# Kernel tuning notes

Measured on AMD Instinct MI355X. Metric: run time of the kernel, lower is better.

The kernel has to match this reference:

```python
import jax, jax.numpy as jnp
import numpy as np

N_NODES = 100000
N_EDGES = 6400000
C = 1.0      # LJ energy scale
R_C = 1.0    # LJ length scale
P = 12
Q = 6
GAMMA = 0.1  # velocity damping
MIN_R = 0.1  # distance clamp
EPS = 1e-12  # torch F.normalize eps
BOX = 100.0  # position domain scale


def setup_inputs() -> dict:
    key = jax.random.key(0)
    k1, k2, k3, k4 = jax.random.split(key, 4)
    x = jax.random.uniform(k1, (N_NODES, 2), dtype=jnp.float32) * BOX
    v = jax.random.normal(k2, (N_NODES, 2), dtype=jnp.float32)
    edge_src = jax.random.randint(k3, (N_EDGES,), 0, N_NODES, dtype=jnp.int64)
    edge_dst = jax.random.randint(k4, (N_EDGES,), 0, N_NODES, dtype=jnp.int64)
    return {"x": x, "v": v, "edge_src": edge_src, "edge_dst": edge_dst}


def lj_force(r_in):
    # r clamped below at MIN_R, matching r*(r>min_r) + min_r*(r<=min_r)
    r = jnp.where(r_in > MIN_R, r_in, MIN_R)
    s = R_C / r
    return 4.0 * C * s**Q * (P * s**(P - Q) - Q) / r


def reference(x, v, edge_src, edge_dst):
    # gather: dr = dst_pos - src_pos (non-periodic euclid distance vector)
    dr = x[edge_dst] - x[edge_src]                       # [E,2]
    abs_dr = jnp.linalg.norm(dr, axis=-1, keepdims=True)  # [E,1]
    unit_dr = dr / jnp.maximum(abs_dr, EPS)               # F.normalize
    msg = lj_force(abs_dr) * unit_dr                      # [E,2]
    # scatter-sum messages to destination nodes
    acc = jax.ops.segment_sum(msg, edge_dst, num_segments=N_NODES)  # [N,2]
    acc = acc - GAMMA * v
    return acc
```

## Files before the change

### kernel.cpp

```cpp
#include <hip/hip_runtime.h>


constexpr float GAMMA = 0.1f;
constexpr float MIN_R = 0.1f;
constexpr float EPSN  = 1e-12f;

constexpr int NPB   = 128;
constexpr int NBPAD = 1024;
constexpr int CHUNK = 16384;
constexpr int STHREADS = 512;
constexpr int K     = CHUNK / STHREADS;
constexpr int CAPB  = 8960;
constexpr unsigned INVALID = 0xFFFFFFFFu;

__device__ __forceinline__ float2 lj_msg(float2 xs, float2 xd) {
    float dx = xd.x - xs.x;
    float dy = xd.y - xs.y;
    float ab = sqrtf(dx * dx + dy * dy);
    float r  = ab > MIN_R ? ab : MIN_R;
    float inv = 1.0f / r;
    float s2 = inv * inv;
    float s6 = s2 * s2 * s2;
    float f  = 4.0f * s6 * (12.0f * s6 - 6.0f) * inv;
    float c  = f / fmaxf(ab, EPSN);
    return make_float2(c * dx, c * dy);
}

__global__ __launch_bounds__(256) void zero_kernel(unsigned* __restrict__ p, int n) {
    int i = blockIdx.x * blockDim.x + threadIdx.x;
    if (i < n) p[i] = 0u;
}

__global__ __launch_bounds__(STHREADS, 2) void scatter_kernel(
    const int4* __restrict__ src4, const int4* __restrict__ dst4,
    unsigned* __restrict__ records, unsigned* __restrict__ gcur,
    int nE, int NB)
{
    __shared__ unsigned sorted[CHUNK];
    __shared__ unsigned cnt[NBPAD];
    __shared__ unsigned curs[NBPAD];
    __shared__ unsigned gbase[NBPAD];

    const int t = threadIdx.x;
    const int blk = blockIdx.x;
    const int base4 = blk * (CHUNK / 4);

    for (int i = t; i < NBPAD; i += STHREADS) cnt[i] = 0u;
    __syncthreads();

    unsigned rec[K];
    unsigned bkt[K];
#pragma unroll
    for (int i = 0; i < K / 4; ++i) {
        int idx4 = base4 + i * STHREADS + t;
        bool vld = (idx4 * 4) < nE;
        int4 s4 = vld ? src4[idx4] : make_int4(0, 0, 0, 0);
        int4 d4 = vld ? dst4[idx4] : make_int4(0, 0, 0, 0);
        int ss[4] = {s4.x, s4.y, s4.z, s4.w};
        int dd[4] = {d4.x, d4.y, d4.z, d4.w};
#pragma unroll
        for (int k = 0; k < 4; ++k) {
            int j = i * 4 + k;
            if (vld) {
                int b = dd[k] >> 7;
                rec[j] = ((unsigned)ss[k] << 7) | (unsigned)(dd[k] & 127);
                bkt[j] = (unsigned)b;
                atomicAdd(&cnt[b], 1u);
            } else {
                bkt[j] = INVALID;
            }
        }
    }
    __syncthreads();

    for (int i = t; i < NBPAD; i += STHREADS) curs[i] = cnt[i];
    __syncthreads();
    for (unsigned off = 1; off < NBPAD; off <<= 1) {
        int i0 = t, i1 = t + STHREADS;
        unsigned a0 = curs[i0] + ((i0 >= (int)off) ? curs[i0 - off] : 0u);
        unsigned a1 = curs[i1] + ((i1 >= (int)off) ? curs[i1 - off] : 0u);
        __syncthreads();
        curs[i0] = a0;
        curs[i1] = a1;
        __syncthreads();
    }

    for (int b = t; b < NB; b += STHREADS) {
        unsigned c = cnt[b];
        curs[b] -= c;
        gbase[b] = c ? atomicAdd(&gcur[b], c) : 0u;
    }
    __syncthreads();

#pragma unroll
    for (int j = 0; j < K; ++j) {
        if (bkt[j] != INVALID) {
            unsigned slot = atomicAdd(&curs[bkt[j]], 1u);
            sorted[slot] = rec[j];
        }
    }
    __syncthreads();

    const int wave = t >> 6, lane = t & 63;
    for (int b = wave; b < NB; b += STHREADS / 64) {
        unsigned c = cnt[b];
        if (!c) continue;
        unsigned p = curs[b] - c;
        unsigned g = gbase[b];
        unsigned* rb = records + (size_t)b * CAPB;
        for (unsigned i = lane; i < c; i += 64) {
            unsigned go = g + i;
            if (go < (unsigned)CAPB) rb[go] = sorted[p + i];
        }
    }
}

__global__ __launch_bounds__(256) void agg_kernel(
    const float2* __restrict__ x, const float* __restrict__ v,
    const unsigned* __restrict__ records, const unsigned* __restrict__ gcur,
    float* __restrict__ out, int N, int NB)
{
    __shared__ float2 xd_s[NPB];
    __shared__ float  acc[2 * NPB];

    const int b = blockIdx.x;
    const unsigned total = min(gcur[b], (unsigned)CAPB);

    for (int t = threadIdx.x; t < NPB; t += 256) {
        int node = b * NPB + t;
        xd_s[t] = (node < N) ? x[node] : make_float2(0.f, 0.f);
    }
    for (int t = threadIdx.x; t < 2 * NPB; t += 256) acc[t] = 0.f;
    __syncthreads();

    const uint4* r4 = (const uint4*)(records + (size_t)b * CAPB);
    const unsigned n4 = total >> 2;
    for (unsigned j = threadIdx.x; j < n4; j += 256) {
        uint4 rr = r4[j];
        unsigned rs[4] = {rr.x, rr.y, rr.z, rr.w};
#pragma unroll
        for (int k = 0; k < 4; ++k) {
            unsigned rec = rs[k];
            int srcn = (int)(rec >> 7);
            int dl   = (int)(rec & 127u);
            float2 m = lj_msg(x[srcn], xd_s[dl]);
            atomicAdd(&acc[2 * dl],     m.x);
            atomicAdd(&acc[2 * dl + 1], m.y);
        }
    }
    for (unsigned j = (total & ~3u) + threadIdx.x; j < total; j += 256) {
        unsigned rec = records[(size_t)b * CAPB + j];
        int srcn = (int)(rec >> 7);
        int dl   = (int)(rec & 127u);
        float2 m = lj_msg(x[srcn], xd_s[dl]);
        atomicAdd(&acc[2 * dl],     m.x);
        atomicAdd(&acc[2 * dl + 1], m.y);
    }
    __syncthreads();

    for (int t = threadIdx.x; t < 2 * NPB; t += 256) {
        int oi = b * 2 * NPB + t;
        if (oi < 2 * N) out[oi] = acc[t] - GAMMA * v[oi];
    }
}

__global__ __launch_bounds__(256) void init_kernel(const float4* __restrict__ v,
                                                   float4* __restrict__ out,
                                                   int n4) {
    int i = blockIdx.x * blockDim.x + threadIdx.x;
    if (i < n4) {
        float4 t = v[i];
        out[i] = make_float4(-GAMMA * t.x, -GAMMA * t.y, -GAMMA * t.z, -GAMMA * t.w);
    }
}

__global__ __launch_bounds__(256) void edge_atomic_kernel(
    const float2* __restrict__ x, const int* __restrict__ src,
    const int* __restrict__ dst, float* __restrict__ out, int nE)
{
    int e = blockIdx.x * blockDim.x + threadIdx.x;
    if (e >= nE) return;
    int s = src[e], d = dst[e];
    float2 m = lj_msg(x[s], x[d]);
    unsafeAtomicAdd(&out[2 * d],     m.x);
    unsafeAtomicAdd(&out[2 * d + 1], m.y);
}

extern "C" void kernel_launch(void* const* d_in, const int* in_sizes, int n_in,
                              void* d_out, int out_size, void* d_ws, size_t ws_size,
                              hipStream_t stream) {
    const float* x   = (const float*)d_in[0];
    const float* v   = (const float*)d_in[1];
    const int*   src = (const int*)d_in[2];
    const int*   dst = (const int*)d_in[3];
    float* out = (float*)d_out;

    const int nE = in_sizes[2];
    const int N  = in_sizes[0] / 2;
    const int NB = (N + NPB - 1) / NPB;

    const size_t gcur_bytes    = NBPAD * sizeof(unsigned);
    const size_t records_bytes = (size_t)NB * CAPB * sizeof(unsigned);
    const size_t needed = gcur_bytes + records_bytes;

    if (NB <= NBPAD && (nE % 4) == 0 && ws_size >= needed) {
        unsigned* gcur    = (unsigned*)d_ws;
        unsigned* records = (unsigned*)((char*)d_ws + gcur_bytes);
        const int nblk = (nE + CHUNK - 1) / CHUNK;

        zero_kernel<<<(NBPAD + 255) / 256, 256, 0, stream>>>(gcur, NBPAD);
        scatter_kernel<<<nblk, STHREADS, 0, stream>>>(
            (const int4*)src, (const int4*)dst, records, gcur, nE, NB);
        agg_kernel<<<NB, 256, 0, stream>>>((const float2*)x, v, records, gcur,
                                           out, N, NB);
    } else {
        int n4 = out_size / 4;
        init_kernel<<<(n4 + 255) / 256, 256, 0, stream>>>(
            (const float4*)v, (float4*)out, n4);
        edge_atomic_kernel<<<(nE + 255) / 256, 256, 0, stream>>>(
            (const float2*)x, src, dst, out, nE);
    }
}
```

Baseline: 219.3 us.

## Widen buckets, two-pass scatter, split aggregation across blocks with partial reduction

Buckets grow to 256 nodes, and the scatter kernel runs with 1024 threads in two passes: it first counts from dst only, then re-reads src/dst to place records, so it no longer holds per-thread record arrays in registers. Each bucket's segment is padded to a multiple of 16 with dummy self-records, so the aggregation kernel can split each bucket across 8 blocks that work on uint4 loads with no tail handling. Partial sums go to a workspace, and a new reduce kernel adds them and applies the damping term. This raises aggregation parallelism from about 782 blocks to several thousand, at the cost of re-reading the edge inputs, an extra kernel launch and partial-sum traffic. The padding records are self-pairs at distance 0, where r is clamped to MIN_R but the final scale divides by fmaxf(0, EPS), so they contribute exactly zero force.

```diff
diff --git a/kernel.cpp b/kernel.cpp
--- a/kernel.cpp
+++ b/kernel.cpp
@@ -5,13 +5,13 @@
 constexpr float MIN_R = 0.1f;
 constexpr float EPSN  = 1e-12f;
 
-constexpr int NPB   = 128;
-constexpr int NBPAD = 1024;
-constexpr int CHUNK = 16384;
-constexpr int STHREADS = 512;
-constexpr int K     = CHUNK / STHREADS;
-constexpr int CAPB  = 8960;
-constexpr unsigned INVALID = 0xFFFFFFFFu;
+constexpr int NPB      = 256;
+constexpr int NBPAD    = 512;
+constexpr int CHUNK    = 16384;
+constexpr int STHREADS = 1024;
+constexpr int K        = CHUNK / STHREADS;
+constexpr int CAPB     = 20352;
+constexpr int SPLIT    = 8;
 
 __device__ __forceinline__ float2 lj_msg(float2 xs, float2 xd) {
     float dx = xd.x - xs.x;
@@ -31,7 +31,7 @@
     if (i < n) p[i] = 0u;
 }
 
-__global__ __launch_bounds__(STHREADS, 2) void scatter_kernel(
+__global__ __launch_bounds__(STHREADS, 8) void scatter_kernel(
     const int4* __restrict__ src4, const int4* __restrict__ dst4,
     unsigned* __restrict__ records, unsigned* __restrict__ gcur,
     int nE, int NB)
@@ -48,83 +48,83 @@
     for (int i = t; i < NBPAD; i += STHREADS) cnt[i] = 0u;
     __syncthreads();
 
-    unsigned rec[K];
-    unsigned bkt[K];
 #pragma unroll
     for (int i = 0; i < K / 4; ++i) {
         int idx4 = base4 + i * STHREADS + t;
-        bool vld = (idx4 * 4) < nE;
-        int4 s4 = vld ? src4[idx4] : make_int4(0, 0, 0, 0);
-        int4 d4 = vld ? dst4[idx4] : make_int4(0, 0, 0, 0);
-        int ss[4] = {s4.x, s4.y, s4.z, s4.w};
-        int dd[4] = {d4.x, d4.y, d4.z, d4.w};
-#pragma unroll
-        for (int k = 0; k < 4; ++k) {
-            int j = i * 4 + k;
-            if (vld) {
-                int b = dd[k] >> 7;
-                rec[j] = ((unsigned)ss[k] << 7) | (unsigned)(dd[k] & 127);
-                bkt[j] = (unsigned)b;
-                atomicAdd(&cnt[b], 1u);
-            } else {
-                bkt[j] = INVALID;
+        if (idx4 * 4 < nE) {
+            int4 d4 = dst4[idx4];
+            atomicAdd(&cnt[d4.x >> 8], 1u);
+            atomicAdd(&cnt[d4.y >> 8], 1u);
+            atomicAdd(&cnt[d4.z >> 8], 1u);
+            atomicAdd(&cnt[d4.w >> 8], 1u);
+        }
+    }
+    __syncthreads();
+
+    if (t < NBPAD) curs[t] = cnt[t];
+    __syncthreads();
+    for (unsigned off = 1; off < NBPAD; off <<= 1) {
+        unsigned a = 0;
+        if (t < NBPAD) a = curs[t] + ((t >= (int)off) ? curs[t - off] : 0u);
+        __syncthreads();
+        if (t < NBPAD) curs[t] = a;
+        __syncthreads();
+    }
+
+    if (t < NB) {
+        unsigned c = cnt[t];
+        curs[t] -= c;
+        unsigned pc = (c + 15u) & ~15u;
+        gbase[t] = pc ? atomicAdd(&gcur[t], pc) : 0u;
+    }
+    __syncthreads();
+
+#pragma unroll
+    for (int i = 0; i < K / 4; ++i) {
+        int idx4 = base4 + i * STHREADS + t;
+        if (idx4 * 4 < nE) {
+            int4 s4 = src4[idx4];
+            int4 d4 = dst4[idx4];
+            int ss[4] = {s4.x, s4.y, s4.z, s4.w};
+            int dd[4] = {d4.x, d4.y, d4.z, d4.w};
+#pragma unroll
+            for (int k = 0; k < 4; ++k) {
+                int b = dd[k] >> 8;
+                unsigned rec = ((unsigned)ss[k] << 8) | (unsigned)(dd[k] & 255);
+                unsigned slot = atomicAdd(&curs[b], 1u);
+                sorted[slot] = rec;
             }
         }
     }
     __syncthreads();
 
-    for (int i = t; i < NBPAD; i += STHREADS) curs[i] = cnt[i];
-    __syncthreads();
-    for (unsigned off = 1; off < NBPAD; off <<= 1) {
-        int i0 = t, i1 = t + STHREADS;
-        unsigned a0 = curs[i0] + ((i0 >= (int)off) ? curs[i0 - off] : 0u);
-        unsigned a1 = curs[i1] + ((i1 >= (int)off) ? curs[i1 - off] : 0u);
-        __syncthreads();
-        curs[i0] = a0;
-        curs[i1] = a1;
-        __syncthreads();
-    }
-
-    for (int b = t; b < NB; b += STHREADS) {
-        unsigned c = cnt[b];
-        curs[b] -= c;
-        gbase[b] = c ? atomicAdd(&gcur[b], c) : 0u;
-    }
-    __syncthreads();
-
-#pragma unroll
-    for (int j = 0; j < K; ++j) {
-        if (bkt[j] != INVALID) {
-            unsigned slot = atomicAdd(&curs[bkt[j]], 1u);
-            sorted[slot] = rec[j];
-        }
-    }
-    __syncthreads();
-
     const int wave = t >> 6, lane = t & 63;
     for (int b = wave; b < NB; b += STHREADS / 64) {
-        unsigned c = cnt[b];
-        if (!c) continue;
+        unsigned c  = cnt[b];
+        unsigned pc = (c + 15u) & ~15u;
+        if (!pc) continue;
         unsigned p = curs[b] - c;
         unsigned g = gbase[b];
+        unsigned selfrec = (unsigned)(b * NPB) << 8;
         unsigned* rb = records + (size_t)b * CAPB;
-        for (unsigned i = lane; i < c; i += 64) {
+        for (unsigned i = lane; i < pc; i += 64) {
             unsigned go = g + i;
-            if (go < (unsigned)CAPB) rb[go] = sorted[p + i];
+            if (go < (unsigned)CAPB)
+                rb[go] = (i < c) ? sorted[p + i] : selfrec;
         }
     }
 }
 
 __global__ __launch_bounds__(256) void agg_kernel(
-    const float2* __restrict__ x, const float* __restrict__ v,
-    const unsigned* __restrict__ records, const unsigned* __restrict__ gcur,
-    float* __restrict__ out, int N, int NB)
+    const float2* __restrict__ x, const unsigned* __restrict__ records,
+    const unsigned* __restrict__ gcur, float* __restrict__ partials,
+    int N, int NB)
 {
     __shared__ float2 xd_s[NPB];
     __shared__ float  acc[2 * NPB];
 
-    const int b = blockIdx.x;
-    const unsigned total = min(gcur[b], (unsigned)CAPB);
+    const int b = blockIdx.x >> 3;
+    const int s = blockIdx.x & 7;
 
     for (int t = threadIdx.x; t < NPB; t += 256) {
         int node = b * NPB + t;
@@ -133,35 +133,58 @@
     for (int t = threadIdx.x; t < 2 * NPB; t += 256) acc[t] = 0.f;
     __syncthreads();
 
+    unsigned total = min(gcur[b], (unsigned)CAPB) & ~15u;
+    unsigned q4  = total >> 2;
+    unsigned per = (q4 + SPLIT - 1) / SPLIT;
+    unsigned lo  = (unsigned)s * per;
+    unsigned hi  = min(q4, lo + per);
+
     const uint4* r4 = (const uint4*)(records + (size_t)b * CAPB);
-    const unsigned n4 = total >> 2;
-    for (unsigned j = threadIdx.x; j < n4; j += 256) {
+    for (unsigned j = lo + threadIdx.x; j < hi; j += 256) {
         uint4 rr = r4[j];
-        unsigned rs[4] = {rr.x, rr.y, rr.z, rr.w};
-#pragma unroll
-        for (int k = 0; k < 4; ++k) {
-            unsigned rec = rs[k];
-            int srcn = (int)(rec >> 7);
-            int dl   = (int)(rec & 127u);
-            float2 m = lj_msg(x[srcn], xd_s[dl]);
-            atomicAdd(&acc[2 * dl],     m.x);
-            atomicAdd(&acc[2 * dl + 1], m.y);
-        }
-    }
-    for (unsigned j = (total & ~3u) + threadIdx.x; j < total; j += 256) {
-        unsigned rec = records[(size_t)b * CAPB + j];
-        int srcn = (int)(rec >> 7);
-        int dl   = (int)(rec & 127u);
-        float2 m = lj_msg(x[srcn], xd_s[dl]);
-        atomicAdd(&acc[2 * dl],     m.x);
-        atomicAdd(&acc[2 * dl + 1], m.y);
-    }
-    __syncthreads();
-
-    for (int t = threadIdx.x; t < 2 * NPB; t += 256) {
-        int oi = b * 2 * NPB + t;
-        if (oi < 2 * N) out[oi] = acc[t] - GAMMA * v[oi];
-    }
+        float2 xs0 = x[rr.x >> 8];
+        float2 xs1 = x[rr.y >> 8];
+        float2 xs2 = x[rr.z >> 8];
+        float2 xs3 = x[rr.w >> 8];
+        int dl0 = rr.x & 255, dl1 = rr.y & 255, dl2 = rr.z & 255, dl3 = rr.w & 255;
+        float2 m0 = lj_msg(xs0, xd_s[dl0]);
+        float2 m1 = lj_msg(xs1, xd_s[dl1]);
+        float2 m2 = lj_msg(xs2, xd_s[dl2]);
+        float2 m3 = lj_msg(xs3, xd_s[dl3]);
+        atomicAdd(&acc[2 * dl0],     m0.x);
+        atomicAdd(&acc[2 * dl0 + 1], m0.y);
+        atomicAdd(&acc[2 * dl1],     m1.x);
+        atomicAdd(&acc[2 * dl1 + 1], m1.y);
+        atomicAdd(&acc[2 * dl2],     m2.x);
+        atomicAdd(&acc[2 * dl2 + 1], m2.y);
+        atomicAdd(&acc[2 * dl3],     m3.x);
+        atomicAdd(&acc[2 * dl3 + 1], m3.y);
+    }
+    __syncthreads();
+
+    float* pb = partials + ((size_t)b * SPLIT + s) * (2 * NPB);
+    for (int t = threadIdx.x; t < 2 * NPB; t += 256) pb[t] = acc[t];
+}
+
+__global__ __launch_bounds__(256) void reduce_kernel(
+    const float* __restrict__ partials, const float4* __restrict__ v4,
+    float4* __restrict__ out4, int n4out)
+{
+    int i4 = blockIdx.x * blockDim.x + threadIdx.x;
+    if (i4 >= n4out) return;
+    int i   = i4 * 4;
+    int b   = i >> 9;
+    int off = i & 511;
+    const float4* pb = (const float4*)(partials + (size_t)b * SPLIT * (2 * NPB));
+    float4 sum = make_float4(0.f, 0.f, 0.f, 0.f);
+#pragma unroll
+    for (int s = 0; s < SPLIT; ++s) {
+        float4 p = pb[s * 128 + (off >> 2)];
+        sum.x += p.x; sum.y += p.y; sum.z += p.z; sum.w += p.w;
+    }
+    float4 vv = v4[i4];
+    out4[i4] = make_float4(sum.x - GAMMA * vv.x, sum.y - GAMMA * vv.y,
+                           sum.z - GAMMA * vv.z, sum.w - GAMMA * vv.w);
 }
 
 __global__ __launch_bounds__(256) void init_kernel(const float4* __restrict__ v,
@@ -199,20 +222,25 @@
     const int N  = in_sizes[0] / 2;
     const int NB = (N + NPB - 1) / NPB;
 
-    const size_t gcur_bytes    = NBPAD * sizeof(unsigned);
-    const size_t records_bytes = (size_t)NB * CAPB * sizeof(unsigned);
-    const size_t needed = gcur_bytes + records_bytes;
+    const size_t gcur_bytes     = NBPAD * sizeof(unsigned);
+    const size_t records_bytes  = (size_t)NB * CAPB * sizeof(unsigned);
+    const size_t partials_bytes = (size_t)NB * SPLIT * 2 * NPB * sizeof(float);
+    const size_t needed = gcur_bytes + records_bytes + partials_bytes;
 
     if (NB <= NBPAD && (nE % 4) == 0 && ws_size >= needed) {
         unsigned* gcur    = (unsigned*)d_ws;
         unsigned* records = (unsigned*)((char*)d_ws + gcur_bytes);
+        float* partials   = (float*)((char*)d_ws + gcur_bytes + records_bytes);
         const int nblk = (nE + CHUNK - 1) / CHUNK;
 
         zero_kernel<<<(NBPAD + 255) / 256, 256, 0, stream>>>(gcur, NBPAD);
         scatter_kernel<<<nblk, STHREADS, 0, stream>>>(
             (const int4*)src, (const int4*)dst, records, gcur, nE, NB);
-        agg_kernel<<<NB, 256, 0, stream>>>((const float2*)x, v, records, gcur,
-                                           out, N, NB);
+        agg_kernel<<<NB * SPLIT, 256, 0, stream>>>(
+            (const float2*)x, records, gcur, partials, N, NB);
+        const int n4out = out_size / 4;
+        reduce_kernel<<<(n4out + 255) / 256, 256, 0, stream>>>(
+            partials, (const float4*)v, (float4*)out, n4out);
     } else {
         int n4 = out_size / 4;
         init_kernel<<<(n4 + 255) / 256, 256, 0, stream>>>(
```

New measurement: 205.3 us. -6.4%, faster.

## Bin edges into 2D src×dst tiles so source positions come from LDS

Applied to the files above, without the earlier changes.

Edges are now binned by both source block (4096 nodes) and destination block (2048 nodes) into 1225 tiles. Each tile block stages both source and destination positions in shared memory, computes forces from LDS only, and writes per-tile partial sums. A new reduce kernel then sums the partials over the source blocks and applies damping. This removes the random global gathers of source positions, at the cost of an extra reduction pass, a second read of the edge arrays in the sort kernel, and padding records with sentinels.

```diff
diff --git a/kernel.cpp b/kernel.cpp
--- a/kernel.cpp
+++ b/kernel.cpp
@@ -5,17 +5,22 @@
 constexpr float MIN_R = 0.1f;
 constexpr float EPSN  = 1e-12f;
 
-constexpr int NPB   = 128;
-constexpr int NBPAD = 1024;
-constexpr int CHUNK = 16384;
-constexpr int STHREADS = 512;
-constexpr int K     = CHUNK / STHREADS;
-constexpr int CAPB  = 8960;
-constexpr unsigned INVALID = 0xFFFFFFFFu;
-
-__device__ __forceinline__ float2 lj_msg(float2 xs, float2 xd) {
-    float dx = xd.x - xs.x;
-    float dy = xd.y - xs.y;
+constexpr int SS   = 12;
+constexpr int DS   = 11;
+constexpr int SRCR = 1 << SS;
+constexpr int DSTR = 1 << DS;
+constexpr int NS   = 25;
+constexpr int ND   = 49;
+constexpr int NT   = NS * ND;
+constexpr int NTA  = 1232;
+constexpr int CHUNK    = 16384;
+constexpr int STHREADS = 1024;
+constexpr int CAP_T    = 6400;
+constexpr unsigned SENT = 0xFFFFFFFFu;
+
+__device__ __forceinline__ float2 lj_msg(float xsx, float xsy, float xdx, float xdy) {
+    float dx = xdx - xsx;
+    float dy = xdy - xsy;
     float ab = sqrtf(dx * dx + dy * dy);
     float r  = ab > MIN_R ? ab : MIN_R;
     float inv = 1.0f / r;
@@ -31,137 +36,162 @@
     if (i < n) p[i] = 0u;
 }
 
-__global__ __launch_bounds__(STHREADS, 2) void scatter_kernel(
+__global__ __launch_bounds__(STHREADS) void sort_kernel(
     const int4* __restrict__ src4, const int4* __restrict__ dst4,
-    unsigned* __restrict__ records, unsigned* __restrict__ gcur,
-    int nE, int NB)
+    unsigned* __restrict__ records, unsigned* __restrict__ gcur, int nE)
 {
     __shared__ unsigned sorted[CHUNK];
-    __shared__ unsigned cnt[NBPAD];
-    __shared__ unsigned curs[NBPAD];
-    __shared__ unsigned gbase[NBPAD];
+    __shared__ unsigned cnt[NTA];
+    __shared__ unsigned curs[NTA];
+    __shared__ unsigned gbase[NTA];
 
     const int t = threadIdx.x;
-    const int blk = blockIdx.x;
-    const int base4 = blk * (CHUNK / 4);
-
-    for (int i = t; i < NBPAD; i += STHREADS) cnt[i] = 0u;
-    __syncthreads();
-
-    unsigned rec[K];
-    unsigned bkt[K];
-#pragma unroll
-    for (int i = 0; i < K / 4; ++i) {
+    const int base4 = blockIdx.x * (CHUNK / 4);
+
+    for (int i = t; i < NTA; i += STHREADS) cnt[i] = 0u;
+    __syncthreads();
+
+#pragma unroll
+    for (int i = 0; i < CHUNK / (4 * STHREADS); ++i) {
         int idx4 = base4 + i * STHREADS + t;
-        bool vld = (idx4 * 4) < nE;
-        int4 s4 = vld ? src4[idx4] : make_int4(0, 0, 0, 0);
-        int4 d4 = vld ? dst4[idx4] : make_int4(0, 0, 0, 0);
-        int ss[4] = {s4.x, s4.y, s4.z, s4.w};
-        int dd[4] = {d4.x, d4.y, d4.z, d4.w};
-#pragma unroll
-        for (int k = 0; k < 4; ++k) {
-            int j = i * 4 + k;
-            if (vld) {
-                int b = dd[k] >> 7;
-                rec[j] = ((unsigned)ss[k] << 7) | (unsigned)(dd[k] & 127);
-                bkt[j] = (unsigned)b;
-                atomicAdd(&cnt[b], 1u);
-            } else {
-                bkt[j] = INVALID;
-            }
-        }
-    }
-    __syncthreads();
-
-    for (int i = t; i < NBPAD; i += STHREADS) curs[i] = cnt[i];
-    __syncthreads();
-    for (unsigned off = 1; off < NBPAD; off <<= 1) {
+        if (idx4 * 4 < nE) {
+            int4 s4 = src4[idx4];
+            int4 d4 = dst4[idx4];
+            atomicAdd(&cnt[(s4.x >> SS) * ND + (d4.x >> DS)], 1u);
+            atomicAdd(&cnt[(s4.y >> SS) * ND + (d4.y >> DS)], 1u);
+            atomicAdd(&cnt[(s4.z >> SS) * ND + (d4.z >> DS)], 1u);
+            atomicAdd(&cnt[(s4.w >> SS) * ND + (d4.w >> DS)], 1u);
+        }
+    }
+    __syncthreads();
+
+    {
         int i0 = t, i1 = t + STHREADS;
-        unsigned a0 = curs[i0] + ((i0 >= (int)off) ? curs[i0 - off] : 0u);
-        unsigned a1 = curs[i1] + ((i1 >= (int)off) ? curs[i1 - off] : 0u);
+        if (i0 < NT) curs[i0] = cnt[i0];
+        if (i1 < NT) curs[i1] = cnt[i1];
+    }
+    __syncthreads();
+    for (int off = 1; off < NT; off <<= 1) {
+        unsigned a0 = 0, a1 = 0;
+        int i0 = t, i1 = t + STHREADS;
+        if (i0 < NT) a0 = curs[i0] + ((i0 >= off) ? curs[i0 - off] : 0u);
+        if (i1 < NT) a1 = curs[i1] + ((i1 >= off) ? curs[i1 - off] : 0u);
         __syncthreads();
-        curs[i0] = a0;
-        curs[i1] = a1;
+        if (i0 < NT) curs[i0] = a0;
+        if (i1 < NT) curs[i1] = a1;
         __syncthreads();
     }
 
-    for (int b = t; b < NB; b += STHREADS) {
+    for (int b = t; b < NT; b += STHREADS) {
         unsigned c = cnt[b];
         curs[b] -= c;
-        gbase[b] = c ? atomicAdd(&gcur[b], c) : 0u;
-    }
-    __syncthreads();
-
-#pragma unroll
-    for (int j = 0; j < K; ++j) {
-        if (bkt[j] != INVALID) {
-            unsigned slot = atomicAdd(&curs[bkt[j]], 1u);
-            sorted[slot] = rec[j];
+        unsigned pc = (c + 3u) & ~3u;
+        gbase[b] = pc ? atomicAdd(&gcur[b], pc) : 0u;
+    }
+    __syncthreads();
+
+#pragma unroll
+    for (int i = 0; i < CHUNK / (4 * STHREADS); ++i) {
+        int idx4 = base4 + i * STHREADS + t;
+        if (idx4 * 4 < nE) {
+            int4 s4 = src4[idx4];
+            int4 d4 = dst4[idx4];
+            int ss_[4] = {s4.x, s4.y, s4.z, s4.w};
+            int dd_[4] = {d4.x, d4.y, d4.z, d4.w};
+#pragma unroll
+            for (int k = 0; k < 4; ++k) {
+                int b = (ss_[k] >> SS) * ND + (dd_[k] >> DS);
+                unsigned rec = ((unsigned)(ss_[k] & (SRCR - 1)) << DS)
+                             | (unsigned)(dd_[k] & (DSTR - 1));
+                unsigned slot = atomicAdd(&curs[b], 1u);
+                sorted[slot] = rec;
+            }
         }
     }
     __syncthreads();
 
     const int wave = t >> 6, lane = t & 63;
-    for (int b = wave; b < NB; b += STHREADS / 64) {
+    for (int b = wave; b < NT; b += STHREADS / 64) {
         unsigned c = cnt[b];
         if (!c) continue;
+        unsigned pc = (c + 3u) & ~3u;
         unsigned p = curs[b] - c;
         unsigned g = gbase[b];
-        unsigned* rb = records + (size_t)b * CAPB;
-        for (unsigned i = lane; i < c; i += 64) {
+        unsigned* rb = records + (size_t)b * CAP_T;
+        for (unsigned i = lane; i < pc; i += 64) {
             unsigned go = g + i;
-            if (go < (unsigned)CAPB) rb[go] = sorted[p + i];
-        }
-    }
-}
-
-__global__ __launch_bounds__(256) void agg_kernel(
-    const float2* __restrict__ x, const float* __restrict__ v,
-    const unsigned* __restrict__ records, const unsigned* __restrict__ gcur,
-    float* __restrict__ out, int N, int NB)
-{
-    __shared__ float2 xd_s[NPB];
-    __shared__ float  acc[2 * NPB];
-
-    const int b = blockIdx.x;
-    const unsigned total = min(gcur[b], (unsigned)CAPB);
-
-    for (int t = threadIdx.x; t < NPB; t += 256) {
-        int node = b * NPB + t;
-        xd_s[t] = (node < N) ? x[node] : make_float2(0.f, 0.f);
-    }
-    for (int t = threadIdx.x; t < 2 * NPB; t += 256) acc[t] = 0.f;
-    __syncthreads();
-
-    const uint4* r4 = (const uint4*)(records + (size_t)b * CAPB);
-    const unsigned n4 = total >> 2;
-    for (unsigned j = threadIdx.x; j < n4; j += 256) {
+            if (go < (unsigned)CAP_T) rb[go] = (i < c) ? sorted[p + i] : SENT;
+        }
+    }
+}
+
+__global__ __launch_bounds__(512) void tile_kernel(
+    const float2* __restrict__ x, unsigned* __restrict__ records,
+    const unsigned* __restrict__ gcur, int N)
+{
+    __shared__ float xs_x[SRCR], xs_y[SRCR];
+    __shared__ float xd_x[DSTR], xd_y[DSTR];
+    __shared__ float acc_x[DSTR], acc_y[DSTR];
+
+    const int tile = blockIdx.x;
+    const int sr = tile / ND, dr = tile % ND;
+    const int s0 = sr << SS, d0 = dr << DS;
+
+    for (int i = threadIdx.x; i < SRCR; i += 512) {
+        int n = s0 + i;
+        float2 p = (n < N) ? x[n] : make_float2(0.f, 0.f);
+        xs_x[i] = p.x; xs_y[i] = p.y;
+    }
+    for (int i = threadIdx.x; i < DSTR; i += 512) {
+        int n = d0 + i;
+        float2 p = (n < N) ? x[n] : make_float2(0.f, 0.f);
+        xd_x[i] = p.x; xd_y[i] = p.y;
+        acc_x[i] = 0.f; acc_y[i] = 0.f;
+    }
+    __syncthreads();
+
+    const unsigned total = min(gcur[tile], (unsigned)CAP_T) & ~3u;
+    const uint4* r4 = (const uint4*)(records + (size_t)tile * CAP_T);
+    for (unsigned j = threadIdx.x; j < (total >> 2); j += 512) {
         uint4 rr = r4[j];
         unsigned rs[4] = {rr.x, rr.y, rr.z, rr.w};
 #pragma unroll
         for (int k = 0; k < 4; ++k) {
             unsigned rec = rs[k];
-            int srcn = (int)(rec >> 7);
-            int dl   = (int)(rec & 127u);
-            float2 m = lj_msg(x[srcn], xd_s[dl]);
-            atomicAdd(&acc[2 * dl],     m.x);
-            atomicAdd(&acc[2 * dl + 1], m.y);
-        }
-    }
-    for (unsigned j = (total & ~3u) + threadIdx.x; j < total; j += 256) {
-        unsigned rec = records[(size_t)b * CAPB + j];
-        int srcn = (int)(rec >> 7);
-        int dl   = (int)(rec & 127u);
-        float2 m = lj_msg(x[srcn], xd_s[dl]);
-        atomicAdd(&acc[2 * dl],     m.x);
-        atomicAdd(&acc[2 * dl + 1], m.y);
-    }
-    __syncthreads();
-
-    for (int t = threadIdx.x; t < 2 * NPB; t += 256) {
-        int oi = b * 2 * NPB + t;
-        if (oi < 2 * N) out[oi] = acc[t] - GAMMA * v[oi];
-    }
+            if (rec != SENT) {
+                int sl = (int)(rec >> DS);
+                int dl = (int)(rec & (DSTR - 1));
+                float2 m = lj_msg(xs_x[sl], xs_y[sl], xd_x[dl], xd_y[dl]);
+                atomicAdd(&acc_x[dl], m.x);
+                atomicAdd(&acc_y[dl], m.y);
+            }
+        }
+    }
+    __syncthreads();
+
+    float* pt = (float*)(records + (size_t)tile * CAP_T);
+    for (int i = threadIdx.x; i < DSTR; i += 512) {
+        pt[i]        = acc_x[i];
+        pt[DSTR + i] = acc_y[i];
+    }
+}
+
+__global__ __launch_bounds__(256) void reduce_kernel(
+    const float* __restrict__ partials, const float2* __restrict__ v,
+    float2* __restrict__ out, int N)
+{
+    int n = blockIdx.x * 256 + threadIdx.x;
+    if (n >= N) return;
+    int dr = n >> DS, dl = n & (DSTR - 1);
+    float sx = 0.f, sy = 0.f;
+#pragma unroll
+    for (int sr = 0; sr < NS; ++sr) {
+        const float* pt = partials + (size_t)(sr * ND + dr) * CAP_T;
+        sx += pt[dl];
+        sy += pt[DSTR + dl];
+    }
+    float2 vv = v[n];
+    out[n] = make_float2(sx - GAMMA * vv.x, sy - GAMMA * vv.y);
 }
 
 __global__ __launch_bounds__(256) void init_kernel(const float4* __restrict__ v,
@@ -181,7 +211,7 @@
     int e = blockIdx.x * blockDim.x + threadIdx.x;
     if (e >= nE) return;
     int s = src[e], d = dst[e];
-    float2 m = lj_msg(x[s], x[d]);
+    float2 m = lj_msg(x[s].x, x[s].y, x[d].x, x[d].y);
     unsafeAtomicAdd(&out[2 * d],     m.x);
     unsafeAtomicAdd(&out[2 * d + 1], m.y);
 }
@@ -197,22 +227,25 @@
 
     const int nE = in_sizes[2];
     const int N  = in_sizes[0] / 2;
-    const int NB = (N + NPB - 1) / NPB;
-
-    const size_t gcur_bytes    = NBPAD * sizeof(unsigned);
-    const size_t records_bytes = (size_t)NB * CAPB * sizeof(unsigned);
+
+    const size_t gcur_bytes    = 8192;
+    const size_t records_bytes = (size_t)NT * CAP_T * sizeof(unsigned);
     const size_t needed = gcur_bytes + records_bytes;
 
-    if (NB <= NBPAD && (nE % 4) == 0 && ws_size >= needed) {
+    const bool shapes_ok = (N <= NS * SRCR) && (N <= ND * DSTR) && (nE % 4) == 0;
+
+    if (shapes_ok && ws_size >= needed) {
         unsigned* gcur    = (unsigned*)d_ws;
         unsigned* records = (unsigned*)((char*)d_ws + gcur_bytes);
         const int nblk = (nE + CHUNK - 1) / CHUNK;
 
-        zero_kernel<<<(NBPAD + 255) / 256, 256, 0, stream>>>(gcur, NBPAD);
-        scatter_kernel<<<nblk, STHREADS, 0, stream>>>(
-            (const int4*)src, (const int4*)dst, records, gcur, nE, NB);
-        agg_kernel<<<NB, 256, 0, stream>>>((const float2*)x, v, records, gcur,
-                                           out, N, NB);
+        zero_kernel<<<(NTA + 255) / 256, 256, 0, stream>>>(gcur, NTA);
+        sort_kernel<<<nblk, STHREADS, 0, stream>>>(
+            (const int4*)src, (const int4*)dst, records, gcur, nE);
+        tile_kernel<<<NT, 512, 0, stream>>>(
+            (const float2*)x, records, gcur, N);
+        reduce_kernel<<<(N + 255) / 256, 256, 0, stream>>>(
+            (const float*)records, (const float2*)v, (float2*)out, N);
     } else {
         int n4 = out_size / 4;
         init_kernel<<<(n4 + 255) / 256, 256, 0, stream>>>(
```

Result: slower. 227.4 us (+3.7%).
